# Kernel optimization log

Hardware: AMD Instinct MI355X
Metric: run time of the kernel (lower is better)

The kernel has to match this reference:

```python
import jax, jax.numpy as jnp
import numpy as np

T = 2048          # num tokens (prefill)
H = 4096          # hidden_size
NH = 32           # num query heads
NKV = 8           # num kv heads (GQA)
HD = H // NH      # head_dim = 128
BASE = 1000000.0  # rope_theta
NEG = -1e30


def _rope(x, positions):
    # NeoX-style rotary embedding (vLLM default). x: [T, nh, HD]
    half = HD // 2
    inv_freq = 1.0 / (BASE ** (jnp.arange(half, dtype=jnp.float32) / half))
    freqs = positions.astype(jnp.float32)[:, None] * inv_freq  # [T, half]
    cos = jnp.concatenate([jnp.cos(freqs), jnp.cos(freqs)], -1)[:, None, :]
    sin = jnp.concatenate([jnp.sin(freqs), jnp.sin(freqs)], -1)[:, None, :]
    rot = jnp.concatenate([-x[..., half:], x[..., :half]], -1)
    return x * cos + rot * sin


def setup_inputs() -> dict:
    key = jax.random.key(0)
    k1, k2, k3 = jax.random.split(key, 3)
    hidden_states = jax.random.normal(k1, (T, H), jnp.float32)
    wqkv = jax.random.normal(k2, (H, (NH + 2 * NKV) * HD), jnp.float32) * 0.02
    wo = jax.random.normal(k3, (NH * HD, H), jnp.float32) * 0.02
    positions = jnp.arange(T, dtype=jnp.int32)
    return {"positions": positions, "hidden_states": hidden_states,
            "wqkv": wqkv, "wo": wo}


def reference(positions, hidden_states, wqkv, wo):
    # fused QKV projection
    qkv = hidden_states @ wqkv                      # [T, (NH+2*NKV)*HD]
    q, k, v = jnp.split(qkv, [NH * HD, NH * HD + NKV * HD], axis=-1)
    q = q.reshape(T, NH, HD)
    k = k.reshape(T, NKV, HD)
    v = v.reshape(T, NKV, HD)
    # inline RoPE on q, k
    q = _rope(q, positions)
    k = _rope(k, positions)
    # GQA: expand kv heads to query heads
    rep = NH // NKV
    k = jnp.repeat(k, rep, axis=1)                  # [T, NH, HD]
    v = jnp.repeat(v, rep, axis=1)
    # causal scaled dot-product attention (prefill path of PagedAttention)
    scores = jnp.einsum('qhd,khd->hqk', q, k) * (HD ** -0.5)  # [NH, T, T]
    causal = positions[:, None] >= positions[None, :]          # [T, T]
    scores = jnp.where(causal[None, :, :], scores, NEG)
    probs = jax.nn.softmax(scores, axis=-1)
    attn = jnp.einsum('hqk,khd->qhd', probs, v).reshape(T, NH * HD)
    return attn @ wo
```

## Files before the change

kernel.cpp:

```cpp
#include <hip/hip_runtime.h>
#include <hip/hip_bf16.h>

typedef __attribute__((ext_vector_type(8))) short bf16x8;
typedef __attribute__((ext_vector_type(4))) float f32x4;
typedef unsigned short u16;

#define T_TOK 2048
#define HID 4096
#define NH 32
#define NKV 8
#define HD 128
#define QKVN 6144
#define KOFF 4096
#define VOFF 5120

static __device__ __forceinline__ float bf2f(u16 x) {
    union { float f; unsigned u; } v; v.u = ((unsigned)x) << 16; return v.f;
}
static __device__ __forceinline__ u16 f2bf(float f) {
    union { float f; unsigned u; } v; v.f = f;
    unsigned u = v.u;
    unsigned r = (u + 0x7fff + ((u >> 16) & 1)) >> 16;
    return (u16)r;
}

static __device__ __forceinline__ void gload16(const u16* g, u16* l) {
    __builtin_amdgcn_global_load_lds((const __attribute__((address_space(1))) void*)g,
                                     (__attribute__((address_space(3))) void*)l, 16, 0, 0);
}

__global__ __launch_bounds__(256) void convk(const float* __restrict__ in, u16* __restrict__ out) {
    int i = blockIdx.x * 256 + threadIdx.x;
    float4 v = ((const float4*)in)[i];
    ushort4 o;
    o.x = f2bf(v.x); o.y = f2bf(v.y); o.z = f2bf(v.z); o.w = f2bf(v.w);
    ((ushort4*)out)[i] = o;
}

__global__ __launch_bounds__(256) void transpk(const float* __restrict__ in, u16* __restrict__ out,
                                               int R, int C) {
    __shared__ float tile[64][65];
    int c0 = blockIdx.x * 64, r0 = blockIdx.y * 64;
    int tid = threadIdx.x;
#pragma unroll
    for (int it = 0; it < 4; ++it) {
        int ci = it * 256 + tid;
        int r = ci >> 4, c4 = (ci & 15) * 4;
        float4 v = *(const float4*)&in[(size_t)(r0 + r) * C + c0 + c4];
        tile[r][c4 + 0] = v.x; tile[r][c4 + 1] = v.y; tile[r][c4 + 2] = v.z; tile[r][c4 + 3] = v.w;
    }
    __syncthreads();
#pragma unroll
    for (int it = 0; it < 4; ++it) {
        int ci = it * 256 + tid;
        int c = ci >> 4, rq = (ci & 15) * 4;
        ushort4 o;
        o.x = f2bf(tile[rq + 0][c]); o.y = f2bf(tile[rq + 1][c]);
        o.z = f2bf(tile[rq + 2][c]); o.w = f2bf(tile[rq + 3][c]);
        *(ushort4*)&out[(size_t)(c0 + c) * R + r0 + rq] = o;
    }
}

template <int BN, int OUTF32>
__global__ __launch_bounds__(512) void gemm8p(const u16* __restrict__ A, const u16* __restrict__ Bt,
                                              void* __restrict__ Cout, int M, int N, int K) {
    constexpr int BM = 256, BK = 32;
    constexpr int WN = BN / 4;
    constexpr int NF = WN / 16;
    constexpr int ACALLS = 2;
    constexpr int BCALLS = BN / 128;
    constexpr int CALLS = ACALLS + BCALLS;
    constexpr int PHASES = (BN == 256) ? 2 : 1;
    constexpr int AFR = 8 / PHASES;
    constexpr int CPP = CALLS / PHASES;
    constexpr int ABUF = BM * BK;
    constexpr int BBUF = BN * BK;
    constexpr int BUFSZ = ABUF + BBUF;

    __shared__ __attribute__((aligned(16))) u16 lds[4 * BUFSZ];

    int bid = blockIdx.x;
    int m0 = (bid & 7) * BM, n0 = (bid >> 3) * BN;
    int tid = threadIdx.x, lane = tid & 63, wid = tid >> 6;
    int wm = wid >> 2, wn = wid & 3;
    int l15 = lane & 15, g4 = lane >> 4;
    int srow = lane >> 2;
    int sslot = (lane & 3) ^ (srow & 3);
    int NK = K / BK;

    auto STAGE = [&](int kt, int c) {
        u16* base = &lds[(kt & 3) * BUFSZ];
        size_t kcol = (size_t)kt * BK + sslot * 8;
        if (c < ACALLS) {
            int ch = wid * ACALLS + c;
            gload16(&A[(size_t)(m0 + ch * 16 + srow) * K + kcol], base + ch * 512);
        } else {
            int ch = wid * BCALLS + (c - ACALLS);
            gload16(&Bt[(size_t)(n0 + ch * 16 + srow) * K + kcol], base + ABUF + ch * 512);
        }
    };

    f32x4 acc[8][NF];
#pragma unroll
    for (int i = 0; i < 8; ++i)
#pragma unroll
        for (int j = 0; j < NF; ++j) acc[i][j] = (f32x4){0.f, 0.f, 0.f, 0.f};

    for (int t = 0; t < 3; ++t)
        for (int c = 0; c < CALLS; ++c) STAGE(t, c);
    asm volatile("s_waitcnt vmcnt(%0)" :: "i"(2 * CALLS) : "memory");
    __builtin_amdgcn_s_barrier();
    __builtin_amdgcn_sched_barrier(0);

    for (int g = 0; g < NK; ++g) {
        const u16* ab = &lds[(g & 3) * BUFSZ];
        const u16* bb = ab + ABUF;
        int swz = (g4 ^ (l15 & 3)) * 8;
#pragma unroll
        for (int p = 0; p < PHASES; ++p) {
            bf16x8 af[AFR], bfr[NF];
#pragma unroll
            for (int i = 0; i < AFR; ++i)
                af[i] = *(const bf16x8*)&ab[(wm * 128 + (p * AFR + i) * 16 + l15) * BK + swz];
#pragma unroll
            for (int j = 0; j < NF; ++j)
                bfr[j] = *(const bf16x8*)&bb[(wn * WN + j * 16 + l15) * BK + swz];
            if (g + 3 < NK) {
#pragma unroll
                for (int c = 0; c < CPP; ++c) STAGE(g + 3, p * CPP + c);
            }
            __builtin_amdgcn_s_barrier();
            __builtin_amdgcn_s_setprio(1);
#pragma unroll
            for (int i = 0; i < AFR; ++i)
#pragma unroll
                for (int j = 0; j < NF; ++j)
                    acc[p * AFR + i][j] =
                        __builtin_amdgcn_mfma_f32_16x16x32_bf16(af[i], bfr[j], acc[p * AFR + i][j], 0, 0, 0);
            __builtin_amdgcn_s_setprio(0);
            if (p == PHASES - 1) {
                if (g < NK - 3)       asm volatile("s_waitcnt vmcnt(%0)" :: "i"(2 * CALLS) : "memory");
                else if (g == NK - 3) asm volatile("s_waitcnt vmcnt(%0)" :: "i"(CALLS) : "memory");
                else if (g == NK - 2) asm volatile("s_waitcnt vmcnt(0)" ::: "memory");
            }
            __builtin_amdgcn_s_barrier();
            __builtin_amdgcn_sched_barrier(0);
        }
    }

#pragma unroll
    for (int mi = 0; mi < 8; ++mi)
#pragma unroll
        for (int j = 0; j < NF; ++j)
#pragma unroll
            for (int i = 0; i < 4; ++i) {
                int row = m0 + wm * 128 + mi * 16 + g4 * 4 + i;
                int col = n0 + wn * WN + j * 16 + l15;
                float v = acc[mi][j][i];
                if (OUTF32) ((float*)Cout)[(size_t)row * N + col] = v;
                else        ((u16*)Cout)[(size_t)row * N + col] = f2bf(v);
            }
}

__global__ __launch_bounds__(256) void ropek(u16* __restrict__ qkvb, const int* __restrict__ positions) {
    __shared__ float cs_[64], sn_[64];
    int t = blockIdx.x;
    float pos = (float)positions[t];
    if (threadIdx.x < 64) {
        int d = threadIdx.x;
        float inv = exp2f(-(float)d * (19.931568569324174f / 64.0f));
        float fr = pos * inv;
        cs_[d] = cosf(fr);
        sn_[d] = sinf(fr);
    }
    __syncthreads();
#pragma unroll
    for (int it = 0; it < 10; ++it) {
        int ci = it * 256 + threadIdx.x;
        int hh = ci >> 6, d = ci & 63;
        int base = (hh < NH) ? hh * HD : KOFF + (hh - NH) * HD;
        size_t off = (size_t)t * QKVN + base + d;
        float x1 = bf2f(qkvb[off]);
        float x2 = bf2f(qkvb[off + 64]);
        float s = sn_[d], c = cs_[d];
        qkvb[off]      = f2bf(x1 * c - x2 * s);
        qkvb[off + 64] = f2bf(x2 * c + x1 * s);
    }
}

__global__ __launch_bounds__(256) void vtranspk(const u16* __restrict__ qkvb, u16* __restrict__ vT) {
    __shared__ __attribute__((aligned(16))) u16 tile[64][136];
    int kvh = blockIdx.x, t0 = blockIdx.y * 64;
    int tid = threadIdx.x;
#pragma unroll
    for (int it = 0; it < 4; ++it) {
        int ci = it * 256 + tid;
        int r = ci >> 4, c8 = (ci & 15) * 8;
        *(bf16x8*)&tile[r][c8] = *(const bf16x8*)&qkvb[(size_t)(t0 + r) * QKVN + VOFF + kvh * HD + c8];
    }
    __syncthreads();
#pragma unroll
    for (int it = 0; it < 4; ++it) {
        int ci = it * 256 + tid;
        int d = ci >> 3, tc = (ci & 7) * 8;
        union { bf16x8 v; u16 u[8]; } o;
#pragma unroll
        for (int e = 0; e < 8; ++e) o.u[e] = tile[tc + e][d];
        *(bf16x8*)&vT[((size_t)kvh * HD + d) * T_TOK + t0 + tc] = o.v;
    }
}

__global__ __launch_bounds__(256) void attnk(const u16* __restrict__ qkvb, const u16* __restrict__ vT,
                                             u16* __restrict__ attnb) {
    __shared__ __attribute__((aligned(16))) u16 kt_[64 * 136];
    __shared__ __attribute__((aligned(16))) u16 vt_[128 * 72];
    __shared__ __attribute__((aligned(16))) u16 pl_[4 * 16 * 72];
    int h = blockIdx.x, qt = 31 - blockIdx.y;
    int kvh = h >> 2;
    int q0 = qt * 64;
    int tid = threadIdx.x, lane = tid & 63, wid = tid >> 6;
    int l15 = lane & 15, g = lane >> 4;
    const float scale = 0.08838834764831845f;

    int kr = tid >> 4, kc = (tid & 15) * 8;
    int vd = tid >> 3, vc = (tid & 7) * 8;
    const u16* kbase = qkvb + KOFF + (size_t)kvh * HD + kc;
    const u16* vbase = vT + ((size_t)kvh * HD) * T_TOK + vc;

    bf16x8 qf[4];
    int qrow = q0 + wid * 16 + l15;
#pragma unroll
    for (int ks = 0; ks < 4; ++ks)
        qf[ks] = *(const bf16x8*)&qkvb[(size_t)qrow * QKVN + h * HD + ks * 32 + g * 8];

    f32x4 o[8];
#pragma unroll
    for (int df = 0; df < 8; ++df) o[df] = (f32x4){0.f, 0.f, 0.f, 0.f};
    float m_run[4], l_run[4];
#pragma unroll
    for (int i = 0; i < 4; ++i) { m_run[i] = -3.0e38f; l_run[i] = 0.f; }

    bf16x8 kreg[4], vreg[4];
#pragma unroll
    for (int it = 0; it < 4; ++it)
        kreg[it] = *(const bf16x8*)&kbase[(size_t)(it * 16 + kr) * QKVN];
#pragma unroll
    for (int it = 0; it < 4; ++it)
        vreg[it] = *(const bf16x8*)&vbase[(size_t)(it * 32 + vd) * T_TOK];
#pragma unroll
    for (int it = 0; it < 4; ++it) *(bf16x8*)&kt_[(it * 16 + kr) * 136 + kc] = kreg[it];
#pragma unroll
    for (int it = 0; it < 4; ++it) *(bf16x8*)&vt_[(it * 32 + vd) * 72 + vc] = vreg[it];
    {
        int ktl = (1 <= qt) ? 1 : qt;
#pragma unroll
        for (int it = 0; it < 4; ++it)
            kreg[it] = *(const bf16x8*)&kbase[(size_t)(ktl * 64 + it * 16 + kr) * QKVN];
#pragma unroll
        for (int it = 0; it < 4; ++it)
            vreg[it] = *(const bf16x8*)&vbase[(size_t)(it * 32 + vd) * T_TOK + ktl * 64];
    }
    __syncthreads();

    for (int kt2 = 0; kt2 <= qt; ++kt2) {
        int kvb = kt2 * 64;

        f32x4 s[4];
#pragma unroll
        for (int nf = 0; nf < 4; ++nf) s[nf] = (f32x4){0.f, 0.f, 0.f, 0.f};
        __builtin_amdgcn_s_setprio(1);
#pragma unroll
        for (int ks = 0; ks < 4; ++ks) {
#pragma unroll
            for (int nf = 0; nf < 4; ++nf) {
                bf16x8 bfr = *(const bf16x8*)&kt_[(nf * 16 + l15) * 136 + ks * 32 + g * 8];
                s[nf] = __builtin_amdgcn_mfma_f32_16x16x32_bf16(qf[ks], bfr, s[nf], 0, 0, 0);
            }
        }
        __builtin_amdgcn_s_setprio(0);

        float mrow[4];
#pragma unroll
        for (int i = 0; i < 4; ++i) {
            int qr = q0 + wid * 16 + g * 4 + i;
            float mx = -3.0e38f;
#pragma unroll
            for (int nf = 0; nf < 4; ++nf) {
                int kvc = kvb + nf * 16 + l15;
                float v = s[nf][i] * scale;
                v = (kvc <= qr) ? v : -1.0e30f;
                s[nf][i] = v;
                mx = fmaxf(mx, v);
            }
            mrow[i] = mx;
        }
#pragma unroll
        for (int dd = 1; dd < 16; dd <<= 1)
#pragma unroll
            for (int i = 0; i < 4; ++i) mrow[i] = fmaxf(mrow[i], __shfl_xor(mrow[i], dd));

        int ok = 1;
#pragma unroll
        for (int i = 0; i < 4; ++i) ok &= (mrow[i] <= m_run[i] + 8.0f) ? 1 : 0;
        if (!__all(ok)) {
            float alpha[4];
#pragma unroll
            for (int i = 0; i < 4; ++i) {
                float mnew = fmaxf(m_run[i], mrow[i]);
                alpha[i] = __expf(m_run[i] - mnew);
                m_run[i] = mnew;
                l_run[i] *= alpha[i];
            }
#pragma unroll
            for (int df = 0; df < 8; ++df)
#pragma unroll
                for (int i = 0; i < 4; ++i) o[df][i] *= alpha[i];
        }

        float rsum[4] = {0.f, 0.f, 0.f, 0.f};
#pragma unroll
        for (int nf = 0; nf < 4; ++nf)
#pragma unroll
            for (int i = 0; i < 4; ++i) {
                float p = __expf(s[nf][i] - m_run[i]);
                rsum[i] += p;
                pl_[wid * 1152 + (g * 4 + i) * 72 + nf * 16 + l15] = f2bf(p);
            }
#pragma unroll
        for (int dd = 1; dd < 16; dd <<= 1)
#pragma unroll
            for (int i = 0; i < 4; ++i) rsum[i] += __shfl_xor(rsum[i], dd);
#pragma unroll
        for (int i = 0; i < 4; ++i) l_run[i] += rsum[i];

        __builtin_amdgcn_s_setprio(1);
#pragma unroll
        for (int ks2 = 0; ks2 < 2; ++ks2) {
            bf16x8 af = *(const bf16x8*)&pl_[wid * 1152 + l15 * 72 + ks2 * 32 + g * 8];
#pragma unroll
            for (int df = 0; df < 8; ++df) {
                bf16x8 bfr = *(const bf16x8*)&vt_[(df * 16 + l15) * 72 + ks2 * 32 + g * 8];
                o[df] = __builtin_amdgcn_mfma_f32_16x16x32_bf16(af, bfr, o[df], 0, 0, 0);
            }
        }
        __builtin_amdgcn_s_setprio(0);

        if (kt2 < qt) {
            __syncthreads();
#pragma unroll
            for (int it = 0; it < 4; ++it) *(bf16x8*)&kt_[(it * 16 + kr) * 136 + kc] = kreg[it];
#pragma unroll
            for (int it = 0; it < 4; ++it) *(bf16x8*)&vt_[(it * 32 + vd) * 72 + vc] = vreg[it];
            int ktl = (kt2 + 2 <= qt) ? kt2 + 2 : qt;
#pragma unroll
            for (int it = 0; it < 4; ++it)
                kreg[it] = *(const bf16x8*)&kbase[(size_t)(ktl * 64 + it * 16 + kr) * QKVN];
#pragma unroll
            for (int it = 0; it < 4; ++it)
                vreg[it] = *(const bf16x8*)&vbase[(size_t)(it * 32 + vd) * T_TOK + ktl * 64];
            __syncthreads();
        }
    }

#pragma unroll
    for (int df = 0; df < 8; ++df)
#pragma unroll
        for (int i = 0; i < 4; ++i) {
            int qr = q0 + wid * 16 + g * 4 + i;
            int col = h * HD + df * 16 + l15;
            attnb[(size_t)qr * (NH * HD) + col] = f2bf(o[df][i] / l_run[i]);
        }
}

extern "C" void kernel_launch(void* const* d_in, const int* in_sizes, int n_in,
                              void* d_out, int out_size, void* d_ws, size_t ws_size,
                              hipStream_t stream) {
    const int*   positions = (const int*)d_in[0];
    const float* hs        = (const float*)d_in[1];
    const float* wqkv      = (const float*)d_in[2];
    const float* wo        = (const float*)d_in[3];
    float* out = (float*)d_out;

    char* ws = (char*)d_ws;
    u16* hsb   = (u16*)(ws);
    u16* wqkvT = (u16*)(ws + 16777216);
    u16* woT   = (u16*)(ws + 16777216 + 50331648);
    u16* qkvb  = (u16*)(ws + 16777216 + 50331648 + 33554432);
    u16* vT    = (u16*)(ws + 16777216 + 50331648 + 33554432 + 25165824);
    u16* attnb = hsb;

    convk<<<8192, 256, 0, stream>>>(hs, hsb);
    transpk<<<dim3(96, 64), 256, 0, stream>>>(wqkv, wqkvT, HID, QKVN);
    transpk<<<dim3(64, 64), 256, 0, stream>>>(wo, woT, HID, HID);

    gemm8p<256, 0><<<dim3(192), 512, 0, stream>>>(hsb, wqkvT, qkvb, T_TOK, QKVN, HID);

    ropek<<<T_TOK, 256, 0, stream>>>(qkvb, positions);

    vtranspk<<<dim3(NKV, 32), 256, 0, stream>>>(qkvb, vT);

    attnk<<<dim3(NH, 32), 256, 0, stream>>>(qkvb, vT, attnb);

    gemm8p<128, 1><<<dim3(256), 512, 0, stream>>>(attnb, woT, out, T_TOK, HID, HID);
}
```

Baseline: 389.3 us.

## Restructure GEMM main loop: one barrier per k-step, reuse B fragments, new LDS swizzle

The bf16 GEMM inner loop is rewritten so each k-step reads the B fragments from LDS once and splits the A fragments into two halves of four. Each half is followed by part of the global-to-LDS prefetch for step g+3 and its MFMAs. The intermediate barriers between phases are removed, leaving a single barrier at the end of each k-step. The LDS XOR swizzle now keys on row bits 1–2 instead of 0–1, in both the store and the read path, to change the bank-conflict pattern. This cuts synchronisation stalls and repeated B loads, but relies on the 4-deep buffer ring staying race-free with fewer barriers.

```diff
diff --git a/kernel.cpp b/kernel.cpp
--- a/kernel.cpp
+++ b/kernel.cpp
@@ -70,9 +70,7 @@
     constexpr int ACALLS = 2;
     constexpr int BCALLS = BN / 128;
     constexpr int CALLS = ACALLS + BCALLS;
-    constexpr int PHASES = (BN == 256) ? 2 : 1;
-    constexpr int AFR = 8 / PHASES;
-    constexpr int CPP = CALLS / PHASES;
+    constexpr int C1 = 2;
     constexpr int ABUF = BM * BK;
     constexpr int BBUF = BN * BK;
     constexpr int BUFSZ = ABUF + BBUF;
@@ -85,7 +83,8 @@
     int wm = wid >> 2, wn = wid & 3;
     int l15 = lane & 15, g4 = lane >> 4;
     int srow = lane >> 2;
-    int sslot = (lane & 3) ^ (srow & 3);
+    int sslot = (lane & 3) ^ ((lane >> 3) & 3);
+    int swz = (g4 ^ ((l15 >> 1) & 3)) * 8;
     int NK = K / BK;
 
     auto STAGE = [&](int kt, int c) {
@@ -115,37 +114,47 @@
     for (int g = 0; g < NK; ++g) {
         const u16* ab = &lds[(g & 3) * BUFSZ];
         const u16* bb = ab + ABUF;
-        int swz = (g4 ^ (l15 & 3)) * 8;
-#pragma unroll
-        for (int p = 0; p < PHASES; ++p) {
-            bf16x8 af[AFR], bfr[NF];
-#pragma unroll
-            for (int i = 0; i < AFR; ++i)
-                af[i] = *(const bf16x8*)&ab[(wm * 128 + (p * AFR + i) * 16 + l15) * BK + swz];
+
+        bf16x8 bfr[NF], af[4];
+#pragma unroll
+        for (int j = 0; j < NF; ++j)
+            bfr[j] = *(const bf16x8*)&bb[(wn * WN + j * 16 + l15) * BK + swz];
+#pragma unroll
+        for (int i = 0; i < 4; ++i)
+            af[i] = *(const bf16x8*)&ab[(wm * 128 + i * 16 + l15) * BK + swz];
+        if (g + 3 < NK) {
+#pragma unroll
+            for (int c = 0; c < C1; ++c) STAGE(g + 3, c);
+        }
+        __builtin_amdgcn_s_setprio(1);
+#pragma unroll
+        for (int i = 0; i < 4; ++i)
 #pragma unroll
             for (int j = 0; j < NF; ++j)
-                bfr[j] = *(const bf16x8*)&bb[(wn * WN + j * 16 + l15) * BK + swz];
-            if (g + 3 < NK) {
-#pragma unroll
-                for (int c = 0; c < CPP; ++c) STAGE(g + 3, p * CPP + c);
-            }
-            __builtin_amdgcn_s_barrier();
-            __builtin_amdgcn_s_setprio(1);
-#pragma unroll
-            for (int i = 0; i < AFR; ++i)
-#pragma unroll
-                for (int j = 0; j < NF; ++j)
-                    acc[p * AFR + i][j] =
-                        __builtin_amdgcn_mfma_f32_16x16x32_bf16(af[i], bfr[j], acc[p * AFR + i][j], 0, 0, 0);
-            __builtin_amdgcn_s_setprio(0);
-            if (p == PHASES - 1) {
-                if (g < NK - 3)       asm volatile("s_waitcnt vmcnt(%0)" :: "i"(2 * CALLS) : "memory");
-                else if (g == NK - 3) asm volatile("s_waitcnt vmcnt(%0)" :: "i"(CALLS) : "memory");
-                else if (g == NK - 2) asm volatile("s_waitcnt vmcnt(0)" ::: "memory");
-            }
-            __builtin_amdgcn_s_barrier();
-            __builtin_amdgcn_sched_barrier(0);
-        }
+                acc[i][j] = __builtin_amdgcn_mfma_f32_16x16x32_bf16(af[i], bfr[j], acc[i][j], 0, 0, 0);
+        __builtin_amdgcn_s_setprio(0);
+
+        bf16x8 af2[4];
+#pragma unroll
+        for (int i = 0; i < 4; ++i)
+            af2[i] = *(const bf16x8*)&ab[(wm * 128 + (4 + i) * 16 + l15) * BK + swz];
+        if (g + 3 < NK) {
+#pragma unroll
+            for (int c = C1; c < CALLS; ++c) STAGE(g + 3, c);
+        }
+        __builtin_amdgcn_s_setprio(1);
+#pragma unroll
+        for (int i = 0; i < 4; ++i)
+#pragma unroll
+            for (int j = 0; j < NF; ++j)
+                acc[4 + i][j] = __builtin_amdgcn_mfma_f32_16x16x32_bf16(af2[i], bfr[j], acc[4 + i][j], 0, 0, 0);
+        __builtin_amdgcn_s_setprio(0);
+
+        if (g < NK - 3)       asm volatile("s_waitcnt vmcnt(%0)" :: "i"(2 * CALLS) : "memory");
+        else if (g == NK - 3) asm volatile("s_waitcnt vmcnt(%0)" :: "i"(CALLS) : "memory");
+        else if (g == NK - 2) asm volatile("s_waitcnt vmcnt(0)" ::: "memory");
+        __builtin_amdgcn_s_barrier();
+        __builtin_amdgcn_sched_barrier(0);
     }
 
 #pragma unroll
```

New measurement: 342.2 us. 12.1% less time.
